# Kernel optimization log

Hardware: AMD Instinct MI355X
Metric: run time of the kernel (lower is better)

The kernel has to match this reference:

```python
import jax, jax.numpy as jnp
import numpy as np

B = 2; H_IMG = 64; W_IMG = 4096
C1, C2 = 16, 32
D_MODEL = 512            # = C2 * (H_IMG // 4) = headdim * (C2 // 4)
HEADDIM = 64; EXPAND = 2; D_STATE = 64; D_CONV = 4
D_INNER = EXPAND * D_MODEL            # 1024
NHEADS = D_INNER // HEADDIM           # 16
CONV_DIM = D_INNER + 2 * D_STATE      # 1152 (x, B, C share the causal conv)
D_IN_PROJ = 2 * D_INNER + 2 * D_STATE + NHEADS   # 2192 (z, xBC, dt)
FF_HID = 2 * D_MODEL                  # feed_forward_expand = 2
NBLK = 2
EPS = 1e-5


def setup_inputs() -> dict:
    ks = iter(jax.random.split(jax.random.key(0), 64))
    def rn(shape, s=0.02):
        return jax.random.normal(next(ks), shape, jnp.float32) * s
    return {
        "image": jax.random.normal(next(ks), (B, 1, H_IMG, W_IMG), jnp.float32),
        "conv1_w": rn((C1, 1, 7, 7), 0.05),
        "bn1_g": jnp.ones((C1,), jnp.float32), "bn1_b": jnp.zeros((C1,), jnp.float32),
        "conv2_w": rn((C2, C1, 7, 7), 0.05),
        "bn2_g": jnp.ones((C2,), jnp.float32), "bn2_b": jnp.zeros((C2,), jnp.float32),
        "ds_w": rn((C2, 1, 1, 1), 0.05),
        "ds_g": jnp.ones((C2,), jnp.float32), "ds_b": jnp.zeros((C2,), jnp.float32),
        "blk_inproj_w": rn((NBLK, D_IN_PROJ, D_MODEL)),
        "blk_conv_w": rn((NBLK, CONV_DIM, D_CONV), 0.2),
        "blk_conv_b": rn((NBLK, CONV_DIM), 0.02),
        "blk_dt_bias": rn((NBLK, NHEADS), 0.5),
        "blk_A_log": jnp.log(jax.random.uniform(next(ks), (NBLK, NHEADS), jnp.float32, 1.0, 16.0)),
        "blk_D": jnp.ones((NBLK, NHEADS), jnp.float32),
        "blk_norm_w": jnp.ones((NBLK, D_INNER), jnp.float32),
        "blk_outproj_w": rn((NBLK, D_MODEL, D_INNER)),
        "blk_bn_g": jnp.ones((NBLK, D_MODEL), jnp.float32), "blk_bn_b": jnp.zeros((NBLK, D_MODEL), jnp.float32),
        "blk_ff_w1": rn((NBLK, FF_HID, D_MODEL)),
        "blk_ff_b1": jnp.zeros((NBLK, FF_HID), jnp.float32),
        "blk_ff_bn1_g": jnp.ones((NBLK, FF_HID), jnp.float32), "blk_ff_bn1_b": jnp.zeros((NBLK, FF_HID), jnp.float32),
        "blk_ff_w2": rn((NBLK, D_MODEL, FF_HID)),
        "blk_ff_b2": jnp.zeros((NBLK, D_MODEL), jnp.float32),
        "blk_ff_bn2_g": jnp.ones((NBLK, D_MODEL), jnp.float32), "blk_ff_bn2_b": jnp.zeros((NBLK, D_MODEL), jnp.float32),
    }


def _conv2d(x, w, stride, pad):
    return jax.lax.conv_general_dilated(x, w, (stride, stride), [(pad, pad), (pad, pad)],
                                        dimension_numbers=("NCHW", "OIHW", "NCHW"))


def _bn(x, g, b, axes):
    # Training-mode batch norm (batch statistics, biased variance), matching torch default train().
    m = jnp.mean(x, axes, keepdims=True)
    v = jnp.var(x, axes, keepdims=True)
    sh = [1] * x.ndim; sh[1] = -1
    return (x - m) * jax.lax.rsqrt(v + EPS) * g.reshape(sh) + b.reshape(sh)


def _mamba2(t, w_in, conv_w, conv_b, dt_bias, A_log, Dp, norm_w, w_out):
    # t: (B, L, d_model). Faithful Mamba2 forward: in_proj -> causal depthwise conv
    # + silu -> selective state-space scan -> D skip -> gated RMSNorm -> out_proj.
    Bsz, L, _ = t.shape
    zxbcdt = jnp.einsum("bld,ed->ble", t, w_in)
    z, xBC, dt = jnp.split(zxbcdt, [D_INNER, D_INNER + CONV_DIM], axis=-1)
    dt = jax.nn.softplus(dt + dt_bias)                          # (B,L,H)
    xp = jnp.pad(xBC, ((0, 0), (D_CONV - 1, 0), (0, 0)))        # causal depthwise conv
    xBC = sum(xp[:, k:k + L, :] * conv_w[:, k] for k in range(D_CONV)) + conv_b
    xBC = jax.nn.silu(xBC)
    x, Bm, Cm = jnp.split(xBC, [D_INNER, D_INNER + D_STATE], axis=-1)
    xh = x.reshape(Bsz, L, NHEADS, HEADDIM)                      # (B,L,H,P)
    dA = jnp.exp(dt * (-jnp.exp(A_log)))                         # (B,L,H)

    def step(h, inp):
        dA_t, dt_t, x_t, B_t, C_t = inp
        h = dA_t[:, :, None, None] * h + jnp.einsum("bh,bhp,bn->bhpn", dt_t, x_t, B_t)
        return h, jnp.einsum("bhpn,bn->bhp", h, C_t)

    h0 = jnp.zeros((Bsz, NHEADS, HEADDIM, D_STATE), t.dtype)
    xs = tuple(jnp.moveaxis(a, 1, 0) for a in (dA, dt, xh, Bm, Cm))
    _, ys = jax.lax.scan(step, h0, xs)                           # ys: (L,B,H,P)
    y = jnp.moveaxis(ys, 0, 1) + xh * Dp[None, None, :, None]
    y = y.reshape(Bsz, L, D_INNER) * jax.nn.silu(z)              # gated RMSNorm
    y = y * jax.lax.rsqrt(jnp.mean(y * y, -1, keepdims=True) + EPS) * norm_w
    return jnp.einsum("ble,de->bld", y, w_out)


def reference(image, conv1_w, bn1_g, bn1_b, conv2_w, bn2_g, bn2_b, ds_w, ds_g, ds_b,
              blk_inproj_w, blk_conv_w, blk_conv_b, blk_dt_bias, blk_A_log, blk_D,
              blk_norm_w, blk_outproj_w, blk_bn_g, blk_bn_b,
              blk_ff_w1, blk_ff_b1, blk_ff_bn1_g, blk_ff_bn1_b,
              blk_ff_w2, blk_ff_b2, blk_ff_bn2_g, blk_ff_bn2_b):
    # Conv stem with stride-4 residual downsample
    h = _bn(_conv2d(image, conv1_w, 2, 3), bn1_g, bn1_b, (0, 2, 3))
    h = _bn(_conv2d(h, conv2_w, 2, 3), bn2_g, bn2_b, (0, 2, 3))
    res = _bn(_conv2d(image, ds_w, 4, 0), ds_g, ds_b, (0, 2, 3))
    h = jax.nn.relu(h + res)
    tokens = h.reshape(h.shape[0], -1, h.shape[-1])              # [B, C*H, W] image_to_sequence
    for i in range(NBLK):
        res = tokens
        t = _mamba2(jnp.swapaxes(tokens, 1, 2), blk_inproj_w[i], blk_conv_w[i], blk_conv_b[i],
                    blk_dt_bias[i], blk_A_log[i], blk_D[i], blk_norm_w[i], blk_outproj_w[i])
        tokens = _bn(jnp.swapaxes(t, 1, 2), blk_bn_g[i], blk_bn_b[i], (0, 2)) + res
        ff_res = tokens
        f = jnp.einsum("bcl,hc->bhl", tokens, blk_ff_w1[i]) + blk_ff_b1[i][None, :, None]
        f = jax.nn.relu(_bn(f, blk_ff_bn1_g[i], blk_ff_bn1_b[i], (0, 2)))
        f = jnp.einsum("bhl,ch->bcl", f, blk_ff_w2[i]) + blk_ff_b2[i][None, :, None]
        tokens = _bn(f, blk_ff_bn2_g[i], blk_ff_bn2_b[i], (0, 2)) + ff_res
    return tokens
```

## Files before the change

kernel.cpp:

```cpp
#include <hip/hip_runtime.h>
#include <cstddef>
#include <cstdint>

static constexpr int L_    = 1024;
static constexpr int DM_   = 512;
static constexpr int EPROJ = 2192;
static constexpr int DI_   = 1024;
static constexpr int CONVD = 1152;
static constexpr int HN_   = 16;
static constexpr int FH_   = 1024;

static constexpr size_t O_CONV1 = 0;
static constexpr size_t O_CONV2 = 2097152;
static constexpr size_t O_TOKA  = O_CONV2 + 1048576;
static constexpr size_t O_TOKB  = O_TOKA + 1048576;
static constexpr size_t O_ZX    = O_TOKB + 1048576;
static constexpr size_t O_XBC   = O_ZX + 4489216;
static constexpr size_t O_DT    = O_XBC + 2359296;
static constexpr size_t O_DA    = O_DT + 32768;
static constexpr size_t O_FFO   = O_DA + 32768;
static constexpr size_t O_STATS = O_FFO + 1048576;
static constexpr size_t STATS_SZ = 16672;
static constexpr size_t O_APROD = O_STATS + STATS_SZ;
static constexpr size_t O_WB    = O_APROD + 256;
static constexpr size_t O_WBB   = O_WB + 14336;
static constexpr size_t O_TABF  = O_WBB + 2695168;
static constexpr size_t O_TBBF  = O_TABF + 524288;

static constexpr size_t WSEG_IN  = 0;
static constexpr size_t WSEG_OUT = 2244608;
static constexpr size_t WSEG_F1  = 3293184;
static constexpr size_t WSEG_F2  = 4341760;
static constexpr size_t WSEG_TOT = 5390336;

__device__ __forceinline__ float sigm(float x) { return 1.f / (1.f + expf(-x)); }

typedef __attribute__((ext_vector_type(8))) short short8;
typedef __attribute__((ext_vector_type(4))) float f32x4;

__device__ __forceinline__ ushort f2bf(float f) {
  union { float f; uint32_t u; } v; v.f = f;
  uint32_t u = v.u;
  return (ushort)((u + 0x7fffu + ((u >> 16) & 1u)) >> 16);
}
__device__ __forceinline__ float bf2f(ushort u) {
  union { uint32_t u; float f; } v; v.u = (uint32_t)u << 16; return v.f;
}
__device__ __forceinline__ uint32_t pk2(float a, float b) {
  return (uint32_t)f2bf(a) | ((uint32_t)f2bf(b) << 16);
}
__device__ __forceinline__ void gl16(const ushort* g, ushort* l) {
  __builtin_amdgcn_global_load_lds(
      (const __attribute__((address_space(1))) void*)g,
      (__attribute__((address_space(3))) void*)l, 16, 0, 0);
}

__global__ __launch_bounds__(256) void prep_k(const float* __restrict__ s0, const float* __restrict__ s1,
                                              const float* __restrict__ s2, const float* __restrict__ s3,
                                              ushort* __restrict__ d,
                                              const float* __restrict__ c2w, ushort* __restrict__ wb,
                                              const float* __restrict__ img, float* __restrict__ imgsums) {
  int bx = blockIdx.x;
  if (bx < 2632) {
    size_t base = ((size_t)bx * 256 + threadIdx.x) * 8;
    const float* s; size_t off;
    if (base < WSEG_OUT)      { s = s0; off = base; }
    else if (base < WSEG_F1)  { s = s1; off = base - WSEG_OUT; }
    else if (base < WSEG_F2)  { s = s2; off = base - WSEG_F1; }
    else                      { s = s3; off = base - WSEG_F2; }
    float4 f0 = *reinterpret_cast<const float4*>(s + off);
    float4 f1 = *reinterpret_cast<const float4*>(s + off + 4);
    uint4 u;
    u.x = pk2(f0.x, f0.y); u.y = pk2(f0.z, f0.w);
    u.z = pk2(f1.x, f1.y); u.w = pk2(f1.z, f1.w);
    *reinterpret_cast<uint4*>(d + base) = u;
  } else if (bx < 2744) {
    int idx = (bx - 2632) * 256 + threadIdx.x;
    int c2 = idx / 896, r = idx % 896;
    int p = r >> 3, kx = r & 7;
    int c1 = p / 7, ky = p - c1 * 7;
    float v = (kx < 7) ? c2w[((size_t)(c2 * 16 + c1) * 7 + ky) * 7 + kx] : 0.f;
    wb[idx] = f2bf(v);
  } else {
    int idx = (bx - 2744) * 256 + threadIdx.x;
    int xx = idx & 1023, yy = (idx >> 10) & 15, b = idx >> 14;
    float v = img[((size_t)b * 64 + yy * 4) * 4096 + xx * 4];
    float s = v, q = v * v;
    for (int o = 32; o > 0; o >>= 1) { s += __shfl_down(s, o); q += __shfl_down(q, o); }
    __shared__ float rs[4], rq[4];
    if ((threadIdx.x & 63) == 0) { rs[threadIdx.x >> 6] = s; rq[threadIdx.x >> 6] = q; }
    __syncthreads();
    if (threadIdx.x == 0) {
      atomicAdd(&imgsums[0], rs[0] + rs[1] + rs[2] + rs[3]);
      atomicAdd(&imgsums[1], rq[0] + rq[1] + rq[2] + rq[3]);
    }
  }
}

__global__ __launch_bounds__(256) void conv1_k(const float* __restrict__ img,
                                               const float* __restrict__ w,
                                               float* __restrict__ out,
                                               float* __restrict__ sums) {
  int idx = blockIdx.x * 256 + threadIdx.x;
  int xq = idx & 511, y = (idx >> 9) & 31, c = (idx >> 14) & 15, b = idx >> 18;
  __shared__ float ws[49];
  if (threadIdx.x < 49) ws[threadIdx.x] = w[c * 49 + threadIdx.x];
  __syncthreads();
  int ix0 = 8 * xq - 3;
  bool fast = (xq > 0) && (xq < 511);
  float acc[4] = {0.f, 0.f, 0.f, 0.f};
  for (int ky = 0; ky < 7; ++ky) {
    int iy = 2 * y - 3 + ky;
    if ((unsigned)iy >= 64u) continue;
    const float* irow = img + ((size_t)b * 64 + iy) * 4096;
    float in[13];
    if (fast) {
      float4 f0 = *reinterpret_cast<const float4*>(&irow[ix0 - 1]);
      float4 f1 = *reinterpret_cast<const float4*>(&irow[ix0 + 3]);
      float4 f2 = *reinterpret_cast<const float4*>(&irow[ix0 + 7]);
      float4 f3 = *reinterpret_cast<const float4*>(&irow[ix0 + 11]);
      in[0] = f0.y; in[1] = f0.z; in[2] = f0.w;
      in[3] = f1.x; in[4] = f1.y; in[5] = f1.z; in[6] = f1.w;
      in[7] = f2.x; in[8] = f2.y; in[9] = f2.z; in[10] = f2.w;
      in[11] = f3.x; in[12] = f3.y;
    } else {
#pragma unroll
      for (int t = 0; t < 13; ++t) {
        int ix = ix0 + t;
        in[t] = ((unsigned)ix < 4096u) ? irow[ix] : 0.f;
      }
    }
#pragma unroll
    for (int kx = 0; kx < 7; ++kx) {
      float wv = ws[ky * 7 + kx];
#pragma unroll
      for (int j = 0; j < 4; ++j) acc[j] += in[2 * j + kx] * wv;
    }
  }
  float4 o; o.x = acc[0]; o.y = acc[1]; o.z = acc[2]; o.w = acc[3];
  *reinterpret_cast<float4*>(&out[(size_t)idx * 4]) = o;
  float s4 = acc[0] + acc[1] + acc[2] + acc[3];
  float q4 = acc[0]*acc[0] + acc[1]*acc[1] + acc[2]*acc[2] + acc[3]*acc[3];
  for (int o2 = 32; o2 > 0; o2 >>= 1) { s4 += __shfl_down(s4, o2); q4 += __shfl_down(q4, o2); }
  __shared__ float rs[4], rq[4];
  if ((threadIdx.x & 63) == 0) { rs[threadIdx.x >> 6] = s4; rq[threadIdx.x >> 6] = q4; }
  __syncthreads();
  if (threadIdx.x == 0) {
    atomicAdd(&sums[c], rs[0] + rs[1] + rs[2] + rs[3]);
    atomicAdd(&sums[16 + c], rq[0] + rq[1] + rq[2] + rq[3]);
  }
}

__global__ __launch_bounds__(256) void conv2_mfma_k(const float* __restrict__ conv1out,
                                                    const float* __restrict__ bn1sums,
                                                    const float* __restrict__ bn1g,
                                                    const float* __restrict__ bn1b,
                                                    const ushort* __restrict__ Wb,
                                                    float* __restrict__ out,
                                                    float* __restrict__ bn2sums) {
  constexpr int RS = 160;
  __shared__ ushort Asub[4 * RS];
  __shared__ ushort Bsub[32 * 40];
  __shared__ float s1l[16], t1l[16];
  __shared__ float cred[64];
  int bid = blockIdx.x;
  int xt = bid & 15, y = (bid >> 4) & 15, b = bid >> 8;
  int x0 = xt * 64;
  int tid = threadIdx.x;
  int wave = tid >> 6, lane = tid & 63;
  int lr = lane >> 4, lc = lane & 15;
  int sr = wave, si = tid & 63;
  if (tid < 16) {
    float mean = bn1sums[tid] * (1.f / 131072.f);
    float var = bn1sums[16 + tid] * (1.f / 131072.f) - mean * mean;
    float s = bn1g[tid] * rsqrtf(var + 1e-5f);
    s1l[tid] = s; t1l[tid] = bn1b[tid] - mean * s;
  }
  if (tid < 64) cred[tid] = 0.f;
  f32x4 acc[2];
  acc[0] = (f32x4){0.f, 0.f, 0.f, 0.f};
  acc[1] = (f32x4){0.f, 0.f, 0.f, 0.f};
  __syncthreads();

  float aval[3];
  uint2 bval;
  auto fetch = [&](int c) {
    bval = *reinterpret_cast<const uint2*>(&Wb[(tid >> 3) * 896 + c * 32 + (tid & 7) * 4]);
    int p = 4 * c + sr;
    int c1 = p / 7, ky = p - c1 * 7;
    int iy = 2 * y - 3 + ky;
    bool rowok = (unsigned)iy < 32u;
    const float* src = conv1out + (((size_t)(b * 16 + c1) * 32 + (rowok ? iy : 0)) * 2048);
    float s1 = s1l[c1], t1v = t1l[c1];
#pragma unroll
    for (int rep = 0; rep < 3; ++rep) {
      int i = si + rep * 64;
      int gx = 2 * x0 + i - 3;
      bool ok = rowok && (i < 134) && ((unsigned)gx < 2048u);
      float raw = src[ok ? gx : 0];
      aval[rep] = ok ? (s1 * raw + t1v) : 0.f;
    }
  };

  fetch(0);
  for (int c = 0; c < 28; ++c) {
    *reinterpret_cast<uint2*>(&Bsub[(tid >> 3) * 40 + (tid & 7) * 4]) = bval;
#pragma unroll
    for (int rep = 0; rep < 3; ++rep) {
      int i = si + rep * 64;
      if (i < RS) Asub[sr * RS + i] = f2bf(aval[rep]);
    }
    __syncthreads();
    if (c + 1 < 28) fetch(c + 1);
    int pos = wave * 16 + lc;
    union { uint32_t u[4]; short8 s; } ua;
    ua.u[0] = *reinterpret_cast<const uint32_t*>(&Asub[lr * RS + 2 * pos + 0]);
    ua.u[1] = *reinterpret_cast<const uint32_t*>(&Asub[lr * RS + 2 * pos + 2]);
    ua.u[2] = *reinterpret_cast<const uint32_t*>(&Asub[lr * RS + 2 * pos + 4]);
    ua.u[3] = *reinterpret_cast<const uint32_t*>(&Asub[lr * RS + 2 * pos + 6]);
    short8 af = ua.s;
    short8 bf0 = *reinterpret_cast<const short8*>(&Bsub[(0 + lc) * 40 + lr * 8]);
    short8 bf1 = *reinterpret_cast<const short8*>(&Bsub[(16 + lc) * 40 + lr * 8]);
    acc[0] = __builtin_amdgcn_mfma_f32_16x16x32_bf16(af, bf0, acc[0], 0, 0, 0);
    acc[1] = __builtin_amdgcn_mfma_f32_16x16x32_bf16(af, bf1, acc[1], 0, 0, 0);
    __syncthreads();
  }
#pragma unroll
  for (int j = 0; j < 2; ++j) {
    int c2 = j * 16 + lc;
    size_t base = (((size_t)(b * 32 + c2)) * 16 + y) * 1024 + x0 + wave * 16 + lr * 4;
#pragma unroll
    for (int r = 0; r < 4; ++r) out[base + r] = acc[j][r];
  }
#pragma unroll
  for (int j = 0; j < 2; ++j) {
    float cs = acc[j][0] + acc[j][1] + acc[j][2] + acc[j][3];
    float cq = acc[j][0]*acc[j][0] + acc[j][1]*acc[j][1] + acc[j][2]*acc[j][2] + acc[j][3]*acc[j][3];
    cs += __shfl_down(cs, 16); cs += __shfl_down(cs, 32);
    cq += __shfl_down(cq, 16); cq += __shfl_down(cq, 32);
    if (lane < 16) { atomicAdd(&cred[j * 16 + lane], cs); atomicAdd(&cred[32 + j * 16 + lane], cq); }
  }
  __syncthreads();
  if (tid < 64) atomicAdd(&bn2sums[tid], cred[tid]);
}

__global__ __launch_bounds__(256) void stem_fuse_k(const float* __restrict__ conv2,
                                                   const float* __restrict__ img,
                                                   const float* __restrict__ bn2sums,
                                                   const float* __restrict__ g2, const float* __restrict__ b2,
                                                   const float* __restrict__ imgsums,
                                                   const float* __restrict__ dsw,
                                                   const float* __restrict__ dsg, const float* __restrict__ dsb,
                                                   float* __restrict__ tok,
                                                   ushort* __restrict__ tok_bf) {
  int idx = blockIdx.x * 256 + threadIdx.x;
  int d = idx & 511, l = (idx >> 9) & 1023, b = idx >> 19;
  int c = d >> 4, hh = d & 15;
  float m2 = bn2sums[c] * (1.f / 32768.f);
  float v2 = bn2sums[32 + c] * (1.f / 32768.f) - m2 * m2;
  float s2 = g2[c] * rsqrtf(v2 + 1e-5f);
  float mi = imgsums[0] * (1.f / 32768.f);
  float vi = imgsums[1] * (1.f / 32768.f) - mi * mi;
  float wv = dsw[c];
  float sd = dsg[c] * rsqrtf(wv * wv * vi + 1e-5f);
  float v = s2 * conv2[((size_t)(b * 32 + c) * 16 + hh) * 1024 + l] + (b2[c] - m2 * s2)
          + (wv * sd) * img[((size_t)b * 64 + hh * 4) * 4096 + l * 4] + (dsb[c] - wv * mi * sd);
  v = fmaxf(v, 0.f);
  tok[idx] = v;
  tok_bf[idx] = f2bf(v);
}

template <int DTEPI>
__global__ __launch_bounds__(256) void gemm64_k(const ushort* __restrict__ A,
                                                const ushort* __restrict__ W,
                                                const float* __restrict__ bias,
                                                ushort* __restrict__ Out,
                                                float* __restrict__ colsums,
                                                int N, int K,
                                                const float* __restrict__ dtb,
                                                const float* __restrict__ alog,
                                                float* __restrict__ dtO,
                                                float* __restrict__ dAO) {
  __shared__ ushort As[4096];
  __shared__ ushort Bs[4096];
  const int tid = threadIdx.x;
  const int GX = gridDim.x;
  int bid = blockIdx.y * GX + blockIdx.x;
  int xcd = bid & 7, slot = bid >> 3;
  const int bm = (xcd * 4 + (slot & 3)) * 64;
  const int bn = (slot >> 2) * 64;
  const int wave = tid >> 6, lane = tid & 63;
  const int lr = lane >> 4, lc = lane & 15;
  const int wmo = (wave >> 1) * 32, wno = (wave & 1) * 32;

  const int q0 = (wave << 6) + lane, q1 = q0 + 256;
  const int r0 = q0 >> 3, g0 = q0 & 7;
  const int r1 = q1 >> 3, g1 = q1 & 7;
  const size_t ar0 = (size_t)(bm + r0) * K + ((g0 ^ (r0 & 7)) << 3);
  const size_t ar1 = (size_t)(bm + r1) * K + ((g1 ^ (r1 & 7)) << 3);
  int wr0 = bn + r0; wr0 = wr0 < N ? wr0 : N - 1;
  int wr1 = bn + r1; wr1 = wr1 < N ? wr1 : N - 1;
  const size_t br0 = (size_t)wr0 * K + ((g0 ^ (r0 & 7)) << 3);
  const size_t br1 = (size_t)wr1 * K + ((g1 ^ (r1 & 7)) << 3);
  ushort* la0 = &As[wave << 9];
  ushort* la1 = &As[2048 + (wave << 9)];
  ushort* lb0 = &Bs[wave << 9];
  ushort* lb1 = &Bs[2048 + (wave << 9)];

  f32x4 acc[2][2];
  acc[0][0] = acc[0][1] = acc[1][0] = acc[1][1] = (f32x4){0.f, 0.f, 0.f, 0.f};

  const int NT = K >> 6;
  for (int t = 0; t < NT; ++t) {
    const int k0 = t << 6;
    gl16(A + ar0 + k0, la0);
    gl16(A + ar1 + k0, la1);
    gl16(W + br0 + k0, lb0);
    gl16(W + br1 + k0, lb1);
    __syncthreads();
#pragma unroll
    for (int ks = 0; ks < 2; ++ks) {
      short8 af[2], bq[2];
#pragma unroll
      for (int i = 0; i < 2; ++i) {
        int row = wmo + i * 16 + lc;
        af[i] = *reinterpret_cast<const short8*>(&As[(row << 6) + ((((ks << 2) + lr) ^ (row & 7)) << 3)]);
      }
#pragma unroll
      for (int j = 0; j < 2; ++j) {
        int row = wno + j * 16 + lc;
        bq[j] = *reinterpret_cast<const short8*>(&Bs[(row << 6) + ((((ks << 2) + lr) ^ (row & 7)) << 3)]);
      }
#pragma unroll
      for (int i = 0; i < 2; ++i)
#pragma unroll
        for (int j = 0; j < 2; ++j)
          acc[i][j] = __builtin_amdgcn_mfma_f32_16x16x32_bf16(af[i], bq[j], acc[i][j], 0, 0, 0);
    }
    __syncthreads();
  }

  float bv[2];
#pragma unroll
  for (int j = 0; j < 2; ++j) {
    int gc = bn + wno + j * 16 + lc;
    bv[j] = (bias && gc < N) ? bias[gc] : 0.f;
  }
  if (colsums) {
#pragma unroll
    for (int j = 0; j < 2; ++j) {
      int gc = bn + wno + j * 16 + lc;
      float cs = 0.f, cq = 0.f;
#pragma unroll
      for (int i = 0; i < 2; ++i)
#pragma unroll
        for (int r = 0; r < 4; ++r) { float o = acc[i][j][r] + bv[j]; cs += o; cq += o * o; }
      cs += __shfl_down(cs, 16); cs += __shfl_down(cs, 32);
      cq += __shfl_down(cq, 16); cq += __shfl_down(cq, 32);
      if (lane < 16 && gc < N) { atomicAdd(&colsums[gc], cs); atomicAdd(&colsums[N + gc], cq); }
    }
  }
  if (DTEPI) {
#pragma unroll
    for (int j = 0; j < 2; ++j) {
      int gc = bn + wno + j * 16 + lc;
      if (gc >= 2176 && gc < 2192) {
        int h = gc - 2176;
        float na = -expf(alog[h]);
        float db = dtb[h];
#pragma unroll
        for (int i = 0; i < 2; ++i)
#pragma unroll
          for (int r = 0; r < 4; ++r) {
            int row = bm + wmo + i * 16 + lr * 4 + r;
            float raw = acc[i][j][r] + db;
            float dt = raw > 20.f ? raw : log1pf(expf(raw));
            dtO[row * 16 + h] = dt;
            dAO[row * 16 + h] = expf(dt * na);
          }
      }
    }
  }
#pragma unroll
  for (int i = 0; i < 2; ++i)
#pragma unroll
    for (int j = 0; j < 2; ++j)
#pragma unroll
      for (int r = 0; r < 4; ++r)
        As[((wmo + i * 16 + lr * 4 + r) << 6) + wno + j * 16 + lc] = f2bf(acc[i][j][r] + bv[j]);
  __syncthreads();
#pragma unroll
  for (int s = 0; s < 2; ++s) {
    int q = tid + s * 256;
    int r = q >> 3, g = q & 7;
    int col = bn + (g << 3);
    if (col < N)
      *reinterpret_cast<uint4*>(Out + (size_t)(bm + r) * N + col) =
          *reinterpret_cast<const uint4*>(&As[(r << 6) + (g << 3)]);
  }
}

__global__ __launch_bounds__(256) void conv_silu_k(const ushort* __restrict__ zx,
                                                   const float* __restrict__ cw,
                                                   const float* __restrict__ cb,
                                                   float* __restrict__ out) {
  int idx = blockIdx.x * 256 + threadIdx.x;
  int c = idx % CONVD;
  int row = idx / CONVD;
  int l = row & 1023, bb = row >> 10;
  float acc = cb[c];
#pragma unroll
  for (int k = 0; k < 4; ++k) {
    int ll = l - 3 + k;
    if (ll >= 0) acc += bf2f(zx[((size_t)(bb * 1024 + ll)) * EPROJ + 1024 + c]) * cw[c * 4 + k];
  }
  out[idx] = acc * sigm(acc);
}

__global__ __launch_bounds__(256) void scan_a_k(const float* __restrict__ xbc,
                                                const float* __restrict__ dtA,
                                                const float* __restrict__ dAA,
                                                float* __restrict__ Hbuf,
                                                float* __restrict__ aprod) {
  constexpr int SCH = 16;
  int bid = blockIdx.x;
  int c  = bid & 7;
  int pg = (bid >> 3) & 3;
  int hh = (bid >> 5) & 15;
  int b  = bid >> 9;
  int tid = threadIdx.x;
  int pl = tid >> 4, nq = tid & 15, n0 = nq * 4;
  int p = pg * 16 + pl;
  __shared__ float sB[2][SCH][64], sx[2][SCH][16];
  __shared__ float sdt[2][SCH], sdA[2][SCH];
  const float* xb = xbc + (size_t)b * L_ * CONVD;
  const float* dtp = dtA + b * (L_ * HN_) + hh;
  const float* dAp = dAA + b * (L_ * HN_) + hh;
  size_t hoff = (((size_t)c * 2 + b) * 16 + hh) * 4096 + (size_t)p * 64 + n0;
  float4 st = make_float4(0.f, 0.f, 0.f, 0.f);
  float ap = 1.f;
  auto stage = [&](int l0, int buf) {
    int ll = tid >> 4, nn = (tid & 15) * 4;
    const float* base = xb + (size_t)(l0 + ll) * CONVD;
    *reinterpret_cast<float4*>(&sB[buf][ll][nn]) = *reinterpret_cast<const float4*>(base + 1024 + nn);
    if (nq < 4)
      *reinterpret_cast<float4*>(&sx[buf][ll][nq * 4]) =
          *reinterpret_cast<const float4*>(base + hh * 64 + pg * 16 + nq * 4);
    else if (nq == 4) sdt[buf][ll] = dtp[(l0 + ll) * HN_];
    else if (nq == 5) sdA[buf][ll] = dAp[(l0 + ll) * HN_];
  };
  int lbase = c * 128;
  stage(lbase, 0);
  int buf = 0;
  for (int s = 0; s < 8; ++s) {
    __syncthreads();
    if (s + 1 < 8) stage(lbase + (s + 1) * SCH, buf ^ 1);
#pragma unroll
    for (int j = 0; j < SCH; ++j) {
      float xv = sx[buf][j][pl];
      float dtv = sdt[buf][j], dAv = sdA[buf][j];
      float4 Bv = *reinterpret_cast<float4*>(&sB[buf][j][n0]);
      float co = dtv * xv;
      st.x = dAv * st.x + co * Bv.x;
      st.y = dAv * st.y + co * Bv.y;
      st.z = dAv * st.z + co * Bv.z;
      st.w = dAv * st.w + co * Bv.w;
      ap *= dAv;
    }
    buf ^= 1;
  }
  *reinterpret_cast<float4*>(&Hbuf[hoff]) = st;
  if (tid == 0) aprod[c * 32 + b * 16 + hh] = ap;
}

__global__ __launch_bounds__(256) void scan_c_k(const float* __restrict__ xbc,
                                                const float* __restrict__ dtA,
                                                const float* __restrict__ dAA,
                                                const float* __restrict__ Dq,
                                                const float* __restrict__ Hbuf,
                                                const float* __restrict__ aprod,
                                                float* __restrict__ y) {
  constexpr int SCH = 16;
  int bid = blockIdx.x;
  int c  = bid & 7;
  int pg = (bid >> 3) & 3;
  int hh = (bid >> 5) & 15;
  int b  = bid >> 9;
  int tid = threadIdx.x;
  int pl = tid >> 4, nq = tid & 15, n0 = nq * 4;
  int p = pg * 16 + pl;
  __shared__ float sB[2][SCH][64], sC[2][SCH][64], sx[2][SCH][16];
  __shared__ float sdt[2][SCH], sdA[2][SCH];
  const float* xb = xbc + (size_t)b * L_ * CONVD;
  const float* dtp = dtA + b * (L_ * HN_) + hh;
  const float* dAp = dAA + b * (L_ * HN_) + hh;
  float* yp_ = y + (size_t)b * L_ * DI_ + hh * 64 + p;
  float Dh = Dq[hh];
  float4 st = make_float4(0.f, 0.f, 0.f, 0.f);
  for (int cc = 0; cc < c; ++cc) {
    float4 he = *reinterpret_cast<const float4*>(
        &Hbuf[(((size_t)cc * 2 + b) * 16 + hh) * 4096 + (size_t)p * 64 + n0]);
    float a = aprod[cc * 32 + b * 16 + hh];
    st.x = a * st.x + he.x;
    st.y = a * st.y + he.y;
    st.z = a * st.z + he.z;
    st.w = a * st.w + he.w;
  }
  auto stage = [&](int l0, int buf) {
    int ll = tid >> 4, nn = (tid & 15) * 4;
    const float* base = xb + (size_t)(l0 + ll) * CONVD;
    *reinterpret_cast<float4*>(&sB[buf][ll][nn]) = *reinterpret_cast<const float4*>(base + 1024 + nn);
    *reinterpret_cast<float4*>(&sC[buf][ll][nn]) = *reinterpret_cast<const float4*>(base + 1088 + nn);
    if (nq < 4)
      *reinterpret_cast<float4*>(&sx[buf][ll][nq * 4]) =
          *reinterpret_cast<const float4*>(base + hh * 64 + pg * 16 + nq * 4);
    else if (nq == 4) sdt[buf][ll] = dtp[(l0 + ll) * HN_];
    else if (nq == 5) sdA[buf][ll] = dAp[(l0 + ll) * HN_];
  };
  int lbase = c * 128;
  stage(lbase, 0);
  int buf = 0;
  for (int s = 0; s < 8; ++s) {
    __syncthreads();
    if (s + 1 < 8) stage(lbase + (s + 1) * SCH, buf ^ 1);
#pragma unroll
    for (int j = 0; j < SCH; ++j) {
      float xv = sx[buf][j][pl];
      float dtv = sdt[buf][j], dAv = sdA[buf][j];
      float4 Bv = *reinterpret_cast<float4*>(&sB[buf][j][n0]);
      float co = dtv * xv;
      st.x = dAv * st.x + co * Bv.x;
      st.y = dAv * st.y + co * Bv.y;
      st.z = dAv * st.z + co * Bv.z;
      st.w = dAv * st.w + co * Bv.w;
      float4 Cv = *reinterpret_cast<float4*>(&sC[buf][j][n0]);
      float yv = st.x * Cv.x + st.y * Cv.y + st.z * Cv.z + st.w * Cv.w;
      yv += __shfl_xor(yv, 1);
      yv += __shfl_xor(yv, 2);
      yv += __shfl_xor(yv, 4);
      yv += __shfl_xor(yv, 8);
      if (nq == 0) yp_[(size_t)(lbase + s * SCH + j) * DI_] = yv + Dh * xv;
    }
    buf ^= 1;
  }
}

__global__ __launch_bounds__(256) void rmsnorm_gate_k(const float* __restrict__ y,
                                                      const ushort* __restrict__ zx,
                                                      const float* __restrict__ nw,
                                                      ushort* __restrict__ out) {
  int row = blockIdx.x;
  const float* yr = y + (size_t)row * DI_;
  const ushort* zr = zx + (size_t)row * EPROJ;
  int d0 = threadIdx.x * 4;
  float4 yv = *reinterpret_cast<const float4*>(&yr[d0]);
  ushort4 zu = *reinterpret_cast<const ushort4*>(&zr[d0]);
  float4 g;
  float z0 = bf2f(zu.x), z1 = bf2f(zu.y), z2 = bf2f(zu.z), z3 = bf2f(zu.w);
  g.x = yv.x * (z0 * sigm(z0));
  g.y = yv.y * (z1 * sigm(z1));
  g.z = yv.z * (z2 * sigm(z2));
  g.w = yv.w * (z3 * sigm(z3));
  float ss = g.x * g.x + g.y * g.y + g.z * g.z + g.w * g.w;
  for (int o = 32; o > 0; o >>= 1) ss += __shfl_down(ss, o);
  __shared__ float r4[4];
  __shared__ float tot;
  if ((threadIdx.x & 63) == 0) r4[threadIdx.x >> 6] = ss;
  __syncthreads();
  if (threadIdx.x == 0) tot = r4[0] + r4[1] + r4[2] + r4[3];
  __syncthreads();
  float rr = rsqrtf(tot * (1.f / DI_) + 1e-5f);
  float4 nwv = *reinterpret_cast<const float4*>(&nw[d0]);
  uint2 o2;
  o2.x = pk2(g.x * rr * nwv.x, g.y * rr * nwv.y);
  o2.y = pk2(g.z * rr * nwv.z, g.w * rr * nwv.w);
  *reinterpret_cast<uint2*>(&out[(size_t)row * DI_ + d0]) = o2;
}

__global__ __launch_bounds__(256) void apply_bn_fin_k(const ushort* __restrict__ X,
                                                      const float* __restrict__ sums,
                                                      const float* __restrict__ g,
                                                      const float* __restrict__ bb,
                                                      const float* __restrict__ res,
                                                      float* __restrict__ out,
                                                      ushort* __restrict__ out_bf,
                                                      int cmask, int C, float inv, int relu) {
  int idx = blockIdx.x * 256 + threadIdx.x;
  int c = idx & cmask;
  float mean = sums[c] * inv;
  float var = sums[C + c] * inv - mean * mean;
  float s = g[c] * rsqrtf(var + 1e-5f);
  float v = s * bf2f(X[idx]) + (bb[c] - mean * s);
  if (res) v += res[idx];
  if (relu) v = fmaxf(v, 0.f);
  if (out) out[idx] = v;
  if (out_bf) out_bf[idx] = f2bf(v);
}

__global__ __launch_bounds__(256) void transpose_bn_k(const ushort* __restrict__ ffo,
                                                      const float* __restrict__ sums,
                                                      const float* __restrict__ g,
                                                      const float* __restrict__ bb,
                                                      const float* __restrict__ res,
                                                      float* __restrict__ out) {
  __shared__ float tile[32][33];
  int bid = blockIdx.x;
  int eb = bid & 15, lb = (bid >> 4) & 31, b = bid >> 9;
  int tx = threadIdx.x & 31, ty = threadIdx.x >> 5;
  int e = eb * 32 + tx;
  float mean = sums[e] * (1.f / 2048.f);
  float var = sums[512 + e] * (1.f / 2048.f) - mean * mean;
  float s = g[e] * rsqrtf(var + 1e-5f);
  float t0 = bb[e] - mean * s;
#pragma unroll
  for (int i = 0; i < 4; ++i) {
    int l = lb * 32 + ty + i * 8;
    size_t off = ((size_t)b * 1024 + l) * 512 + e;
    tile[ty + i * 8][tx] = s * bf2f(ffo[off]) + t0 + res[off];
  }
  __syncthreads();
#pragma unroll
  for (int i = 0; i < 4; ++i) {
    int e2 = eb * 32 + ty + i * 8;
    out[((size_t)b * 512 + e2) * 1024 + lb * 32 + tx] = tile[tx][ty + i * 8];
  }
}

extern "C" void kernel_launch(void* const* d_in, const int* in_sizes, int n_in,
                              void* d_out, int out_size, void* d_ws, size_t ws_size,
                              hipStream_t stream) {
  const float* img      = (const float*)d_in[0];
  const float* conv1_w  = (const float*)d_in[1];
  const float* bn1_g    = (const float*)d_in[2];
  const float* bn1_b    = (const float*)d_in[3];
  const float* conv2_w  = (const float*)d_in[4];
  const float* bn2_g    = (const float*)d_in[5];
  const float* bn2_b    = (const float*)d_in[6];
  const float* ds_w     = (const float*)d_in[7];
  const float* ds_g     = (const float*)d_in[8];
  const float* ds_b     = (const float*)d_in[9];
  const float* inproj_w = (const float*)d_in[10];
  const float* convw    = (const float*)d_in[11];
  const float* convb    = (const float*)d_in[12];
  const float* dt_bias  = (const float*)d_in[13];
  const float* A_log    = (const float*)d_in[14];
  const float* Dp       = (const float*)d_in[15];
  const float* norm_w   = (const float*)d_in[16];
  const float* outproj_w= (const float*)d_in[17];
  const float* bno_g    = (const float*)d_in[18];
  const float* bno_b    = (const float*)d_in[19];
  const float* ff_w1    = (const float*)d_in[20];
  const float* ff_b1    = (const float*)d_in[21];
  const float* ff1_g    = (const float*)d_in[22];
  const float* ff1_b    = (const float*)d_in[23];
  const float* ff_w2    = (const float*)d_in[24];
  const float* ff_b2    = (const float*)d_in[25];
  const float* ff2_g    = (const float*)d_in[26];
  const float* ff2_b    = (const float*)d_in[27];

  float* w = (float*)d_ws;
  float* stats = w + O_STATS;
  float* st_bn1 = stats + 0;
  float* st_bn2 = stats + 32;
  float* st_img = stats + 96;
  float* aprodp = w + O_APROD;
  ushort* wbp = (ushort*)(w + O_WB);
  ushort* WBB = (ushort*)(w + O_WBB);

  float* tokA = w + O_TOKA;
  float* tokB = w + O_TOKB;
  ushort* tokA_bf = (ushort*)(w + O_TABF);
  ushort* tokB_bf = (ushort*)(w + O_TBBF);
  ushort* zx_bf   = (ushort*)(w + O_ZX);
  float* xbc  = w + O_XBC;
  float* dtA  = w + O_DT;
  float* dAA  = w + O_DA;
  float* Hbuf = w + O_FFO;
  float* y    = w + O_CONV1;
  ushort* y_bf    = (ushort*)(w + O_CONV2);
  ushort* proj_bf = (ushort*)(w + O_ZX);
  ushort* ffh_bf  = (ushort*)(w + O_CONV1);
  ushort* ffo_bf  = (ushort*)(w + O_CONV1 + 1048576);

  hipMemsetAsync(stats, 0, STATS_SZ * sizeof(float), stream);

  prep_k<<<2872, 256, 0, stream>>>(inproj_w, outproj_w, ff_w1, ff_w2, WBB,
                                   conv2_w, wbp, img, st_img);
  conv1_k<<<2048, 256, 0, stream>>>(img, conv1_w, w + O_CONV1, st_bn1);
  conv2_mfma_k<<<512, 256, 0, stream>>>(w + O_CONV1, st_bn1, bn1_g, bn1_b, wbp,
                                        w + O_CONV2, st_bn2);
  stem_fuse_k<<<4096, 256, 0, stream>>>(w + O_CONV2, img, st_bn2, bn2_g, bn2_b,
                                        st_img, ds_w, ds_g, ds_b, tokA, tokA_bf);

  for (int i = 0; i < 2; ++i) {
    float* stb = stats + 288 + i * 8192;
    const ushort* win_i  = WBB + WSEG_IN  + (size_t)i * 1122304;
    const ushort* wout_i = WBB + WSEG_OUT + (size_t)i * 524288;
    const ushort* wff1_i = WBB + WSEG_F1  + (size_t)i * 524288;
    const ushort* wff2_i = WBB + WSEG_F2  + (size_t)i * 524288;

    gemm64_k<1><<<dim3(35, 32), 256, 0, stream>>>(
        tokA_bf, win_i, nullptr, zx_bf, nullptr, EPROJ, DM_,
        dt_bias + i * 16, A_log + i * 16, dtA, dAA);
    conv_silu_k<<<9216, 256, 0, stream>>>(zx_bf, convw + i * CONVD * 4, convb + i * CONVD, xbc);
    scan_a_k<<<1024, 256, 0, stream>>>(xbc, dtA, dAA, Hbuf, aprodp);
    scan_c_k<<<1024, 256, 0, stream>>>(xbc, dtA, dAA, Dp + i * 16, Hbuf, aprodp, y);
    rmsnorm_gate_k<<<2048, 256, 0, stream>>>(y, zx_bf, norm_w + i * DI_, y_bf);
    gemm64_k<0><<<dim3(8, 32), 256, 0, stream>>>(
        y_bf, wout_i, nullptr, proj_bf, stb, DM_, DI_,
        nullptr, nullptr, nullptr, nullptr);
    apply_bn_fin_k<<<4096, 256, 0, stream>>>(proj_bf, stb, bno_g + i * DM_, bno_b + i * DM_,
                                             tokA, tokB, tokB_bf, DM_ - 1, DM_, 1.f / 2048.f, 0);
    gemm64_k<0><<<dim3(16, 32), 256, 0, stream>>>(
        tokB_bf, wff1_i, ff_b1 + i * FH_, ffh_bf, stb + 2048, FH_, DM_,
        nullptr, nullptr, nullptr, nullptr);
    apply_bn_fin_k<<<8192, 256, 0, stream>>>(ffh_bf, stb + 2048, ff1_g + i * FH_, ff1_b + i * FH_,
                                             nullptr, nullptr, ffh_bf, FH_ - 1, FH_, 1.f / 2048.f, 1);
    gemm64_k<0><<<dim3(8, 32), 256, 0, stream>>>(
        ffh_bf, wff2_i, ff_b2 + i * DM_, ffo_bf, stb + 6144, DM_, FH_,
        nullptr, nullptr, nullptr, nullptr);
    if (i == 0)
      apply_bn_fin_k<<<4096, 256, 0, stream>>>(ffo_bf, stb + 6144, ff2_g, ff2_b,
                                               tokB, tokA, tokA_bf, DM_ - 1, DM_, 1.f / 2048.f, 0);
  }
  transpose_bn_k<<<1024, 256, 0, stream>>>(ffo_bf, stats + 288 + 8192 + 6144,
                                           ff2_g + DM_, ff2_b + DM_, tokB, (float*)d_out);
}
```

Before: 485.6 us.

## Restructure chunked SSM scan into local scan plus inter-chunk correction pass

Replaces the two-pass scan (state pass, then full output pass seeded with carried-in state) with a single local pass per chunk that writes outputs, chunk-end states and cumulative decay products. A new correction kernel then adds C·(carried state)·cumA to each output row for chunks 1–7. This avoids running the sequential recurrence twice over the whole sequence. The cost is an extra read-modify-write of y and a cumA buffer placed in the tokA_bf workspace region. Separately, the causal conv+SiLU kernel is vectorized so each thread handles four channels with wide loads and stores.

```diff
diff --git a/kernel.cpp b/kernel.cpp
--- a/kernel.cpp
+++ b/kernel.cpp
@@ -400,85 +400,46 @@
   }
 }
 
-__global__ __launch_bounds__(256) void conv_silu_k(const ushort* __restrict__ zx,
-                                                   const float* __restrict__ cw,
-                                                   const float* __restrict__ cb,
-                                                   float* __restrict__ out) {
+__global__ __launch_bounds__(256) void conv_silu4_k(const ushort* __restrict__ zx,
+                                                    const float* __restrict__ cw,
+                                                    const float* __restrict__ cb,
+                                                    float* __restrict__ out) {
   int idx = blockIdx.x * 256 + threadIdx.x;
-  int c = idx % CONVD;
-  int row = idx / CONVD;
+  int idx4 = idx * 4;
+  int c0 = idx4 % CONVD;
+  int row = idx4 / CONVD;
   int l = row & 1023, bb = row >> 10;
-  float acc = cb[c];
+  float4 w0 = *reinterpret_cast<const float4*>(&cw[(c0 + 0) * 4]);
+  float4 w1 = *reinterpret_cast<const float4*>(&cw[(c0 + 1) * 4]);
+  float4 w2 = *reinterpret_cast<const float4*>(&cw[(c0 + 2) * 4]);
+  float4 w3 = *reinterpret_cast<const float4*>(&cw[(c0 + 3) * 4]);
+  float4 acc = *reinterpret_cast<const float4*>(&cb[c0]);
 #pragma unroll
   for (int k = 0; k < 4; ++k) {
     int ll = l - 3 + k;
-    if (ll >= 0) acc += bf2f(zx[((size_t)(bb * 1024 + ll)) * EPROJ + 1024 + c]) * cw[c * 4 + k];
-  }
-  out[idx] = acc * sigm(acc);
+    if (ll < 0) continue;
+    ushort4 xu = *reinterpret_cast<const ushort4*>(&zx[((size_t)(bb * 1024 + ll)) * EPROJ + 1024 + c0]);
+    float wk0 = (&w0.x)[k], wk1 = (&w1.x)[k], wk2 = (&w2.x)[k], wk3 = (&w3.x)[k];
+    acc.x += bf2f(xu.x) * wk0;
+    acc.y += bf2f(xu.y) * wk1;
+    acc.z += bf2f(xu.z) * wk2;
+    acc.w += bf2f(xu.w) * wk3;
+  }
+  float4 o;
+  o.x = acc.x * sigm(acc.x);
+  o.y = acc.y * sigm(acc.y);
+  o.z = acc.z * sigm(acc.z);
+  o.w = acc.w * sigm(acc.w);
+  *reinterpret_cast<float4*>(&out[idx4]) = o;
 }
 
 __global__ __launch_bounds__(256) void scan_a_k(const float* __restrict__ xbc,
                                                 const float* __restrict__ dtA,
                                                 const float* __restrict__ dAA,
+                                                const float* __restrict__ Dq,
                                                 float* __restrict__ Hbuf,
-                                                float* __restrict__ aprod) {
-  constexpr int SCH = 16;
-  int bid = blockIdx.x;
-  int c  = bid & 7;
-  int pg = (bid >> 3) & 3;
-  int hh = (bid >> 5) & 15;
-  int b  = bid >> 9;
-  int tid = threadIdx.x;
-  int pl = tid >> 4, nq = tid & 15, n0 = nq * 4;
-  int p = pg * 16 + pl;
-  __shared__ float sB[2][SCH][64], sx[2][SCH][16];
-  __shared__ float sdt[2][SCH], sdA[2][SCH];
-  const float* xb = xbc + (size_t)b * L_ * CONVD;
-  const float* dtp = dtA + b * (L_ * HN_) + hh;
-  const float* dAp = dAA + b * (L_ * HN_) + hh;
-  size_t hoff = (((size_t)c * 2 + b) * 16 + hh) * 4096 + (size_t)p * 64 + n0;
-  float4 st = make_float4(0.f, 0.f, 0.f, 0.f);
-  float ap = 1.f;
-  auto stage = [&](int l0, int buf) {
-    int ll = tid >> 4, nn = (tid & 15) * 4;
-    const float* base = xb + (size_t)(l0 + ll) * CONVD;
-    *reinterpret_cast<float4*>(&sB[buf][ll][nn]) = *reinterpret_cast<const float4*>(base + 1024 + nn);
-    if (nq < 4)
-      *reinterpret_cast<float4*>(&sx[buf][ll][nq * 4]) =
-          *reinterpret_cast<const float4*>(base + hh * 64 + pg * 16 + nq * 4);
-    else if (nq == 4) sdt[buf][ll] = dtp[(l0 + ll) * HN_];
-    else if (nq == 5) sdA[buf][ll] = dAp[(l0 + ll) * HN_];
-  };
-  int lbase = c * 128;
-  stage(lbase, 0);
-  int buf = 0;
-  for (int s = 0; s < 8; ++s) {
-    __syncthreads();
-    if (s + 1 < 8) stage(lbase + (s + 1) * SCH, buf ^ 1);
-#pragma unroll
-    for (int j = 0; j < SCH; ++j) {
-      float xv = sx[buf][j][pl];
-      float dtv = sdt[buf][j], dAv = sdA[buf][j];
-      float4 Bv = *reinterpret_cast<float4*>(&sB[buf][j][n0]);
-      float co = dtv * xv;
-      st.x = dAv * st.x + co * Bv.x;
-      st.y = dAv * st.y + co * Bv.y;
-      st.z = dAv * st.z + co * Bv.z;
-      st.w = dAv * st.w + co * Bv.w;
-      ap *= dAv;
-    }
-    buf ^= 1;
-  }
-  *reinterpret_cast<float4*>(&Hbuf[hoff]) = st;
-  if (tid == 0) aprod[c * 32 + b * 16 + hh] = ap;
-}
-
-__global__ __launch_bounds__(256) void scan_c_k(const float* __restrict__ xbc,
-                                                const float* __restrict__ dtA,
-                                                const float* __restrict__ dAA,
-                                                const float* __restrict__ Dq,
-                                                const float* __restrict__ Hbuf,
-                                                const float* __restrict__ aprod,
+                                                float* __restrict__ aprod,
+                                                float* __restrict__ cumA,
                                                 float* __restrict__ y) {
   constexpr int SCH = 16;
   int bid = blockIdx.x;
@@ -496,16 +457,9 @@
   const float* dAp = dAA + b * (L_ * HN_) + hh;
   float* yp_ = y + (size_t)b * L_ * DI_ + hh * 64 + p;
   float Dh = Dq[hh];
+  size_t hoff = (((size_t)c * 2 + b) * 16 + hh) * 4096 + (size_t)p * 64 + n0;
   float4 st = make_float4(0.f, 0.f, 0.f, 0.f);
-  for (int cc = 0; cc < c; ++cc) {
-    float4 he = *reinterpret_cast<const float4*>(
-        &Hbuf[(((size_t)cc * 2 + b) * 16 + hh) * 4096 + (size_t)p * 64 + n0]);
-    float a = aprod[cc * 32 + b * 16 + hh];
-    st.x = a * st.x + he.x;
-    st.y = a * st.y + he.y;
-    st.z = a * st.z + he.z;
-    st.w = a * st.w + he.w;
-  }
+  float ap = 1.f;
   auto stage = [&](int l0, int buf) {
     int ll = tid >> 4, nn = (tid & 15) * 4;
     const float* base = xb + (size_t)(l0 + ll) * CONVD;
@@ -533,6 +487,7 @@
       st.y = dAv * st.y + co * Bv.y;
       st.z = dAv * st.z + co * Bv.z;
       st.w = dAv * st.w + co * Bv.w;
+      ap *= dAv;
       float4 Cv = *reinterpret_cast<float4*>(&sC[buf][j][n0]);
       float yv = st.x * Cv.x + st.y * Cv.y + st.z * Cv.z + st.w * Cv.w;
       yv += __shfl_xor(yv, 1);
@@ -540,8 +495,70 @@
       yv += __shfl_xor(yv, 4);
       yv += __shfl_xor(yv, 8);
       if (nq == 0) yp_[(size_t)(lbase + s * SCH + j) * DI_] = yv + Dh * xv;
+      if (pg == 0 && tid == 0)
+        cumA[(((b << 10) + lbase + s * SCH + j) << 4) + hh] = ap;
     }
     buf ^= 1;
+  }
+  *reinterpret_cast<float4*>(&Hbuf[hoff]) = st;
+  if (pg == 0 && tid == 0) aprod[c * 32 + b * 16 + hh] = ap;
+}
+
+__global__ __launch_bounds__(128) void scan_fix_k(const float* __restrict__ xbc,
+                                                  const float* __restrict__ Hbuf,
+                                                  const float* __restrict__ aprod,
+                                                  const float* __restrict__ cumA,
+                                                  float* __restrict__ y) {
+  __shared__ float hin[64 * 64];
+  int bid = blockIdx.x;
+  int b = bid / 112, rem = bid % 112, hh = rem / 7, c = rem % 7 + 1;
+  int tid = threadIdx.x;
+  {
+    int p = tid >> 1, hf = tid & 1;
+    f32x4 hreg[8];
+#pragma unroll
+    for (int q = 0; q < 8; ++q) hreg[q] = (f32x4){0.f, 0.f, 0.f, 0.f};
+    for (int cc = 0; cc < c; ++cc) {
+      float a = aprod[cc * 32 + b * 16 + hh];
+      const float* src = Hbuf + (((size_t)cc * 2 + b) * 16 + hh) * 4096 + p * 64 + hf * 32;
+#pragma unroll
+      for (int q = 0; q < 8; ++q) {
+        f32x4 v = *reinterpret_cast<const f32x4*>(src + q * 4);
+        hreg[q] = a * hreg[q] + v;
+      }
+    }
+#pragma unroll
+    for (int q = 0; q < 8; ++q) {
+      int g = hf * 8 + q;
+      *reinterpret_cast<f32x4*>(&hin[p * 64 + ((g ^ (p & 15)) << 2)]) = hreg[q];
+    }
+  }
+  __syncthreads();
+  int t = tid;
+  int l = c * 128 + t;
+  const float* crow = xbc + ((size_t)(b * 1024 + l)) * CONVD + 1088;
+  f32x4 C[16];
+#pragma unroll
+  for (int g = 0; g < 16; ++g) C[g] = *reinterpret_cast<const f32x4*>(crow + g * 4);
+  float cum = cumA[(((b << 10) + l) << 4) + hh];
+  float* yrow = y + ((size_t)(b * 1024 + l)) * DI_ + hh * 64;
+  for (int p4 = 0; p4 < 16; ++p4) {
+    int p0 = p4 * 4;
+    f32x4 a0 = {0.f,0.f,0.f,0.f}, a1 = {0.f,0.f,0.f,0.f};
+    f32x4 a2 = {0.f,0.f,0.f,0.f}, a3 = {0.f,0.f,0.f,0.f};
+#pragma unroll
+    for (int g = 0; g < 16; ++g) {
+      a0 += C[g] * *reinterpret_cast<const f32x4*>(&hin[(p0 + 0) * 64 + ((g ^ ((p0 + 0) & 15)) << 2)]);
+      a1 += C[g] * *reinterpret_cast<const f32x4*>(&hin[(p0 + 1) * 64 + ((g ^ ((p0 + 1) & 15)) << 2)]);
+      a2 += C[g] * *reinterpret_cast<const f32x4*>(&hin[(p0 + 2) * 64 + ((g ^ ((p0 + 2) & 15)) << 2)]);
+      a3 += C[g] * *reinterpret_cast<const f32x4*>(&hin[(p0 + 3) * 64 + ((g ^ ((p0 + 3) & 15)) << 2)]);
+    }
+    float4 yv = *reinterpret_cast<float4*>(&yrow[p0]);
+    yv.x += cum * (a0[0] + a0[1] + a0[2] + a0[3]);
+    yv.y += cum * (a1[0] + a1[1] + a1[2] + a1[3]);
+    yv.z += cum * (a2[0] + a2[1] + a2[2] + a2[3]);
+    yv.w += cum * (a3[0] + a3[1] + a3[2] + a3[3]);
+    *reinterpret_cast<float4*>(&yrow[p0]) = yv;
   }
 }
 
@@ -676,6 +693,7 @@
   float* dtA  = w + O_DT;
   float* dAA  = w + O_DA;
   float* Hbuf = w + O_FFO;
+  float* cumA = w + O_TABF;
   float* y    = w + O_CONV1;
   ushort* y_bf    = (ushort*)(w + O_CONV2);
   ushort* proj_bf = (ushort*)(w + O_ZX);
@@ -702,9 +720,9 @@
     gemm64_k<1><<<dim3(35, 32), 256, 0, stream>>>(
         tokA_bf, win_i, nullptr, zx_bf, nullptr, EPROJ, DM_,
         dt_bias + i * 16, A_log + i * 16, dtA, dAA);
-    conv_silu_k<<<9216, 256, 0, stream>>>(zx_bf, convw + i * CONVD * 4, convb + i * CONVD, xbc);
-    scan_a_k<<<1024, 256, 0, stream>>>(xbc, dtA, dAA, Hbuf, aprodp);
-    scan_c_k<<<1024, 256, 0, stream>>>(xbc, dtA, dAA, Dp + i * 16, Hbuf, aprodp, y);
+    conv_silu4_k<<<2304, 256, 0, stream>>>(zx_bf, convw + i * CONVD * 4, convb + i * CONVD, xbc);
+    scan_a_k<<<1024, 256, 0, stream>>>(xbc, dtA, dAA, Dp + i * 16, Hbuf, aprodp, cumA, y);
+    scan_fix_k<<<224, 128, 0, stream>>>(xbc, Hbuf, aprodp, cumA, y);
     rmsnorm_gate_k<<<2048, 256, 0, stream>>>(y, zx_bf, norm_w + i * DI_, y_bf);
     gemm64_k<0><<<dim3(8, 32), 256, 0, stream>>>(
         y_bf, wout_i, nullptr, proj_bf, stb, DM_, DI_,
```

Result: slower. 524.0 us (+7.9%).
